# Performance work log

Measured on AMD Instinct MI355X. Metric: run time of the kernel, lower is better.

Reference implementation:

```python
import jax, jax.numpy as jnp
import numpy as np

N = 50000      # nodes
E = 800000     # edges (avg degree 16)
NFEAT = 256
NHID = 128
NCLASS = 40
NLAYERS_MID = 13  # gc2..gc14


def setup_inputs() -> dict:
    key = jax.random.key(0)
    ks = jax.random.split(key, 16)
    stdv_h = 1.0 / np.sqrt(NHID)     # GraphConvolution stdv = 1/sqrt(out_features)
    stdv_c = 1.0 / np.sqrt(NCLASS)
    u = lambda k, shape, s: jax.random.uniform(k, shape, jnp.float32, -s, s)
    return {
        "x": jax.random.normal(ks[0], (N, NFEAT), jnp.float32),
        "edge_src": jax.random.randint(ks[1], (E,), 0, N, jnp.int32),
        "edge_dst": jax.random.randint(ks[2], (E,), 0, N, jnp.int32),
        "edge_weight": jax.random.uniform(ks[3], (E,), jnp.float32),
        # skip-branch linear (self.weight / self.bias)
        "W0": u(ks[4], (NFEAT, NHID), stdv_h),
        "b0": u(ks[5], (NHID,), stdv_h),
        # gc1: nfeat -> nhid
        "W1": u(ks[6], (NFEAT, NHID), stdv_h),
        "b1": u(ks[7], (NHID,), stdv_h),
        # gc2..gc14: nhid -> nhid, stacked
        "Wmid": u(ks[8], (NLAYERS_MID, NHID, NHID), stdv_h),
        "bmid": u(ks[9], (NLAYERS_MID, NHID), stdv_h),
        # gc15: 14*nhid -> nclass
        "W15": u(ks[10], (14 * NHID, NCLASS), stdv_c),
        "b15": u(ks[11], (NCLASS,), stdv_c),
    }


def reference(x, edge_src, edge_dst, edge_weight, W0, b0, W1, b1, Wmid, bmid, W15, b15):
    n = x.shape[0]

    def gcn(h, W, b):
        # support = h @ W ; out = spmm(adj, support) + b  (adj as weighted edge list)
        support = h @ W
        msgs = support[edge_src] * edge_weight[:, None]           # [E, d]
        agg = jax.ops.segment_sum(msgs, edge_dst, num_segments=n)  # [N, d]
        return agg + b

    z = x @ W0 + b0
    x1 = jax.nn.relu(gcn(x, W1, b1)) + z

    def step(h, Wb):
        W, b = Wb
        hn = jax.nn.relu(gcn(h, W, b)) + h
        return hn, hn

    _, xs = jax.lax.scan(step, x1, (Wmid, bmid))   # xs: [13, N, NHID] = x2..x14
    all_x = jnp.concatenate([x1[None], xs], axis=0)  # [14, N, NHID] = x1..x14
    # concat order in torch code: (x14, x13, ..., x1)
    x_cat = jnp.swapaxes(all_x[::-1], 0, 1).reshape(n, 14 * NHID)
    # dropout is identity in eval mode
    x15 = gcn(x_cat, W15, b15)
    return jax.nn.log_softmax(x15, axis=1)
```

## Files before the change

### kernel.cpp

```cpp
#include <hip/hip_runtime.h>
#include <stdint.h>

#define NN 50000
#define EE 800000
#define DH 128
#define NC 40
#define KCAT (14*DH)
#define CAP 64

typedef __bf16 bf16x8 __attribute__((ext_vector_type(8)));
typedef float floatx4 __attribute__((ext_vector_type(4)));

__device__ __forceinline__ float bf2f(unsigned short u) {
  union { uint32_t i; float f; } v; v.i = ((uint32_t)u) << 16; return v.f;
}
__device__ __forceinline__ unsigned short f2bf(float f) {
  union { float f; uint32_t i; } v; v.f = f;
  uint32_t x = v.i;
  uint32_t r = (x + 0x7fffu + ((x >> 16) & 1u)) >> 16;
  return (unsigned short)r;
}

__global__ void zero_i32(int* p, int n) {
  int i = blockIdx.x * blockDim.x + threadIdx.x;
  if (i < n) p[i] = 0;
}

__global__ void detect_dtype(const unsigned short* xw, int* wildcnt) {
  int t = threadIdx.x;
  int wild = 0;
  for (int i = t; i < 4096; i += 256) {
    unsigned e = (xw[i] >> 7) & 0xFF;
    if (e >= 0x90) wild++;
  }
  if (wild) atomicAdd(wildcnt, wild);
}

__global__ void convert_f(const void* in, unsigned short* outp, int n, const int* flag) {
  bool isf32 = (*flag) > 32;
  for (int i = blockIdx.x * blockDim.x + threadIdx.x; i < n;
       i += gridDim.x * blockDim.x) {
    outp[i] = isf32 ? f2bf(((const float*)in)[i]) : ((const unsigned short*)in)[i];
  }
}

__global__ void transpose_w(const void* B, unsigned short* BT,
                            int L, int K, int M, int Mpad, const int* flag) {
  bool isf32 = (*flag) > 32;
  int total = L * Mpad * K;
  for (int idx = blockIdx.x * blockDim.x + threadIdx.x; idx < total;
       idx += gridDim.x * blockDim.x) {
    int k = idx % K;
    int n = (idx / K) % Mpad;
    int l = idx / (K * Mpad);
    unsigned short v = 0;
    if (n < M) {
      size_t si = (size_t)l * K * M + (size_t)k * M + n;
      v = isf32 ? f2bf(((const float*)B)[si]) : ((const unsigned short*)B)[si];
    }
    BT[idx] = v;
  }
}

__global__ void build_ell(const int* __restrict__ src, const int* __restrict__ dst,
                          const void* __restrict__ w,
                          int* __restrict__ cnt, int2* __restrict__ ell,
                          const int* __restrict__ flag) {
  bool isf32 = (*flag) > 32;
  int e = blockIdx.x * blockDim.x + threadIdx.x;
  if (e >= EE) return;
  int d = dst[e];
  if ((unsigned)d >= NN) return;
  int p = atomicAdd(&cnt[d], 1);
  if (p >= CAP) return;
  int s = src[e];
  float wf = isf32 ? ((const float*)w)[e] : bf2f(((const unsigned short*)w)[e]);
  if ((unsigned)s >= NN) { s = 0; wf = 0.f; }
  union { float f; int i; } wv; wv.f = wf;
  ell[(size_t)d * CAP + p] = make_int2(s, wv.i);
}

__global__ __launch_bounds__(256) void gemm_h(
    const unsigned short* __restrict__ A, int lda,
    const unsigned short* __restrict__ BT, int K,
    unsigned short* __restrict__ C, const unsigned short* __restrict__ bias) {
  __shared__ unsigned short As[128][40];
  __shared__ unsigned short Bs[128][40];
  int t = threadIdx.x;
  int wave = t >> 6, lane = t & 63;
  int wy = wave >> 1, wx = wave & 1;
  int q = lane >> 4, mn = lane & 15;
  int r0 = blockIdx.x * 128;
  floatx4 acc[4][4];
  floatx4 zf = {0.f, 0.f, 0.f, 0.f};
  #pragma unroll
  for (int i = 0; i < 4; ++i)
    #pragma unroll
    for (int j = 0; j < 4; ++j) acc[i][j] = zf;

  int arow = t >> 2;
  int akc = (t & 3) << 3;

  for (int k0 = 0; k0 < K; k0 += 32) {
    #pragma unroll
    for (int h = 0; h < 2; ++h) {
      int r = arow + h * 64;
      uint4 v = make_uint4(0, 0, 0, 0);
      if (r0 + r < NN) v = *(const uint4*)(A + (size_t)(r0 + r) * lda + k0 + akc);
      *(uint4*)(&As[r][akc]) = v;
    }
    #pragma unroll
    for (int h = 0; h < 2; ++h) {
      int n = arow + h * 64;
      uint4 v = *(const uint4*)(BT + (size_t)n * K + k0 + akc);
      *(uint4*)(&Bs[n][akc]) = v;
    }
    __syncthreads();
    bf16x8 fa[4], fb[4];
    #pragma unroll
    for (int i = 0; i < 4; ++i) fa[i] = *(const bf16x8*)(&As[wy * 64 + i * 16 + mn][q * 8]);
    #pragma unroll
    for (int j = 0; j < 4; ++j) fb[j] = *(const bf16x8*)(&Bs[wx * 64 + j * 16 + mn][q * 8]);
    #pragma unroll
    for (int i = 0; i < 4; ++i)
      #pragma unroll
      for (int j = 0; j < 4; ++j)
        acc[i][j] = __builtin_amdgcn_mfma_f32_16x16x32_bf16(fa[i], fb[j], acc[i][j], 0, 0, 0);
    __syncthreads();
  }
  #pragma unroll
  for (int i = 0; i < 4; ++i) {
    int rbase = r0 + wy * 64 + i * 16 + q * 4;
    #pragma unroll
    for (int j = 0; j < 4; ++j) {
      int col = wx * 64 + j * 16 + mn;
      float badd = bias ? bf2f(bias[col]) : 0.0f;
      #pragma unroll
      for (int rr = 0; rr < 4; ++rr) {
        int row = rbase + rr;
        if (row < NN) C[(size_t)row * 128 + col] = f2bf(acc[i][j][rr] + badd);
      }
    }
  }
}

__global__ __launch_bounds__(256) void gemm_cat(
    const unsigned short* __restrict__ A, const unsigned short* __restrict__ BT ,
    float* __restrict__ C) {
  __shared__ unsigned short As[128][40];
  __shared__ unsigned short Bs[48][40];
  int t = threadIdx.x;
  int wave = t >> 6, lane = t & 63;
  int q = lane >> 4, mn = lane & 15;
  int r0 = blockIdx.x * 128;
  floatx4 acc[2][3];
  floatx4 zf = {0.f, 0.f, 0.f, 0.f};
  #pragma unroll
  for (int i = 0; i < 2; ++i)
    #pragma unroll
    for (int j = 0; j < 3; ++j) acc[i][j] = zf;

  int arow = t >> 2;
  int akc = (t & 3) << 3;

  for (int k0 = 0; k0 < KCAT; k0 += 32) {
    #pragma unroll
    for (int h = 0; h < 2; ++h) {
      int r = arow + h * 64;
      uint4 v = make_uint4(0, 0, 0, 0);
      if (r0 + r < NN) v = *(const uint4*)(A + (size_t)(r0 + r) * KCAT + k0 + akc);
      *(uint4*)(&As[r][akc]) = v;
    }
    if (t < 192) {
      uint4 v = *(const uint4*)(BT + (size_t)arow * KCAT + k0 + akc);
      *(uint4*)(&Bs[arow][akc]) = v;
    }
    __syncthreads();
    bf16x8 fa[2], fb[3];
    #pragma unroll
    for (int i = 0; i < 2; ++i) fa[i] = *(const bf16x8*)(&As[wave * 32 + i * 16 + mn][q * 8]);
    #pragma unroll
    for (int j = 0; j < 3; ++j) fb[j] = *(const bf16x8*)(&Bs[j * 16 + mn][q * 8]);
    #pragma unroll
    for (int i = 0; i < 2; ++i)
      #pragma unroll
      for (int j = 0; j < 3; ++j)
        acc[i][j] = __builtin_amdgcn_mfma_f32_16x16x32_bf16(fa[i], fb[j], acc[i][j], 0, 0, 0);
    __syncthreads();
  }
  #pragma unroll
  for (int i = 0; i < 2; ++i) {
    int rbase = r0 + wave * 32 + i * 16 + q * 4;
    #pragma unroll
    for (int j = 0; j < 3; ++j) {
      int col = j * 16 + mn;
      #pragma unroll
      for (int rr = 0; rr < 4; ++rr) {
        int row = rbase + rr;
        if (row < NN && col < NC) C[(size_t)row * NC + col] = acc[i][j][rr];
      }
    }
  }
}

__global__ __launch_bounds__(256) void spmm_layer(
    const unsigned short* __restrict__ support, const int* __restrict__ cnt,
    const int2* __restrict__ ell, const unsigned short* __restrict__ bias,
    const unsigned short* __restrict__ res, int res_stride,
    unsigned short* __restrict__ out, int out_stride) {
  int wave = threadIdx.x >> 6, lane = threadIdx.x & 63;
  int row = blockIdx.x * 4 + wave;
  if (row >= NN) return;
  int n = cnt[row];
  if (n > CAP) n = CAP;
  int2 ev = ell[(size_t)row * CAP + lane];
  float a0 = 0.f, a1 = 0.f;
  int j = 0;
  for (; j + 8 <= n; j += 8) {
    uint32_t g[8];
    int sidx[8];
    #pragma unroll
    for (int u = 0; u < 8; ++u) sidx[u] = __shfl(ev.x, j + u);
    #pragma unroll
    for (int u = 0; u < 8; ++u)
      g[u] = *(const uint32_t*)(support + (size_t)sidx[u] * DH + 2 * lane);
    #pragma unroll
    for (int u = 0; u < 8; ++u) {
      union { int i; float f; } wv; wv.i = __shfl(ev.y, j + u);
      a0 += wv.f * bf2f((unsigned short)(g[u] & 0xffff));
      a1 += wv.f * bf2f((unsigned short)(g[u] >> 16));
    }
  }
  for (; j < n; ++j) {
    int s = __shfl(ev.x, j);
    union { int i; float f; } wv; wv.i = __shfl(ev.y, j);
    uint32_t g = *(const uint32_t*)(support + (size_t)s * DH + 2 * lane);
    a0 += wv.f * bf2f((unsigned short)(g & 0xffff));
    a1 += wv.f * bf2f((unsigned short)(g >> 16));
  }
  uint32_t bw = *(const uint32_t*)(bias + 2 * lane);
  uint32_t rw = *(const uint32_t*)(res + (size_t)row * res_stride + 2 * lane);
  float v0 = fmaxf(a0 + bf2f((unsigned short)(bw & 0xffff)), 0.f) +
             bf2f((unsigned short)(rw & 0xffff));
  float v1 = fmaxf(a1 + bf2f((unsigned short)(bw >> 16)), 0.f) +
             bf2f((unsigned short)(rw >> 16));
  uint32_t o = (uint32_t)f2bf(v0) | ((uint32_t)f2bf(v1) << 16);
  *(uint32_t*)(out + (size_t)row * out_stride + 2 * lane) = o;
}

__global__ __launch_bounds__(256) void spmm_softmax_out(
    const float* __restrict__ s15, const int* __restrict__ cnt,
    const int2* __restrict__ ell, const unsigned short* __restrict__ bias,
    float* __restrict__ out) {
  int wave = threadIdx.x >> 6, lane = threadIdx.x & 63;
  int row = blockIdx.x * 4 + wave;
  if (row >= NN) return;
  int n = cnt[row];
  if (n > CAP) n = CAP;
  int2 ev = ell[(size_t)row * CAP + lane];
  int fl = lane < NC ? lane : NC - 1;
  float acc = 0.f;
  int j = 0;
  for (; j + 4 <= n; j += 4) {
    float g[4];
    #pragma unroll
    for (int u = 0; u < 4; ++u) {
      int s = __shfl(ev.x, j + u);
      g[u] = s15[(size_t)s * NC + fl];
    }
    #pragma unroll
    for (int u = 0; u < 4; ++u) {
      union { int i; float f; } wv; wv.i = __shfl(ev.y, j + u);
      acc += wv.f * g[u];
    }
  }
  for (; j < n; ++j) {
    int s = __shfl(ev.x, j);
    union { int i; float f; } wv; wv.i = __shfl(ev.y, j);
    acc += wv.f * s15[(size_t)s * NC + fl];
  }
  acc += bf2f(bias[fl]);
  float v = (lane < NC) ? acc : -3.0e38f;
  float m = v;
  #pragma unroll
  for (int off = 32; off > 0; off >>= 1) m = fmaxf(m, __shfl_xor(m, off));
  float e = (lane < NC) ? expf(v - m) : 0.f;
  float sum = e;
  #pragma unroll
  for (int off = 32; off > 0; off >>= 1) sum += __shfl_xor(sum, off);
  if (lane < NC) out[(size_t)row * NC + lane] = v - m - logf(sum);
}

extern "C" void kernel_launch(void* const* d_in, const int* in_sizes, int n_in,
                              void* d_out, int out_size, void* d_ws, size_t ws_size,
                              hipStream_t stream) {
  const void* x   = d_in[0];
  const int* esrc = (const int*)d_in[1];
  const int* edst = (const int*)d_in[2];
  const void* ew  = d_in[3];
  const void* W0  = d_in[4];
  const void* b0  = d_in[5];
  const void* W1  = d_in[6];
  const void* b1  = d_in[7];
  const void* Wm  = d_in[8];
  const void* bm  = d_in[9];
  const void* W15 = d_in[10];
  const void* b15 = d_in[11];
  float* out = (float*)d_out;

  char* ws = (char*)d_ws;
  size_t off = 0;
  auto alloc = [&](size_t bytes) -> void* {
    void* p = ws + off;
    off = (off + bytes + 255) & ~(size_t)255;
    return p;
  };
  unsigned short* xcat = (unsigned short*)alloc((size_t)NN * KCAT * 2);
  unsigned short* xbf  = (unsigned short*)alloc((size_t)NN * 256 * 2);
  unsigned short* supp = (unsigned short*)alloc((size_t)NN * DH * 2);
  unsigned short* zbuf = (unsigned short*)alloc((size_t)NN * DH * 2);
  float* s15           = (float*)alloc((size_t)NN * NC * 4);
  int* counts          = (int*)alloc((size_t)(NN + 1) * 4);
  int2* ell            = (int2*)alloc((size_t)NN * CAP * 8);
  unsigned short* W0T  = (unsigned short*)alloc((size_t)256 * 128 * 2);
  unsigned short* W1T  = (unsigned short*)alloc((size_t)256 * 128 * 2);
  unsigned short* WmT  = (unsigned short*)alloc((size_t)13 * 128 * 128 * 2);
  unsigned short* W15T = (unsigned short*)alloc((size_t)48 * 1792 * 2);
  unsigned short* bb   = (unsigned short*)alloc((size_t)(128 + 128 + 13 * 128 + 40) * 2);
  if (off > ws_size) return;
  int* flag = counts + NN;
  unsigned short* b0b  = bb;
  unsigned short* b1b  = bb + 128;
  unsigned short* bmb  = bb + 256;
  unsigned short* b15b = bb + 256 + 13 * 128;

  zero_i32<<<197, 256, 0, stream>>>(counts, NN + 1);
  detect_dtype<<<1, 256, 0, stream>>>((const unsigned short*)x, flag);
  transpose_w<<<128, 256, 0, stream>>>(W0, W0T, 1, 256, 128, 128, flag);
  transpose_w<<<128, 256, 0, stream>>>(W1, W1T, 1, 256, 128, 128, flag);
  transpose_w<<<832, 256, 0, stream>>>(Wm, WmT, 13, 128, 128, 128, flag);
  transpose_w<<<336, 256, 0, stream>>>(W15, W15T, 1, 1792, 40, 48, flag);
  convert_f<<<2048, 256, 0, stream>>>(x, xbf, NN * 256, flag);
  convert_f<<<1, 128, 0, stream>>>(b0, b0b, 128, flag);
  convert_f<<<1, 128, 0, stream>>>(b1, b1b, 128, flag);
  convert_f<<<7, 256, 0, stream>>>(bm, bmb, 13 * 128, flag);
  convert_f<<<1, 64, 0, stream>>>(b15, b15b, 40, flag);
  build_ell<<<3125, 256, 0, stream>>>(esrc, edst, ew, counts, ell, flag);

  int gb = (NN + 127) / 128;
  int sb = (NN + 3) / 4;
  gemm_h<<<gb, 256, 0, stream>>>(xbf, 256, W0T, 256, zbuf, b0b);
  gemm_h<<<gb, 256, 0, stream>>>(xbf, 256, W1T, 256, supp, nullptr);
  spmm_layer<<<sb, 256, 0, stream>>>(supp, counts, ell, b1b, zbuf, DH,
                                     xcat + 13 * DH, KCAT);
  for (int l = 0; l < 13; ++l) {
    gemm_h<<<gb, 256, 0, stream>>>(xcat + (13 - l) * DH, KCAT, WmT + l * 128 * 128, 128,
                                   supp, nullptr);
    spmm_layer<<<sb, 256, 0, stream>>>(supp, counts, ell, bmb + l * DH,
                                       xcat + (13 - l) * DH, KCAT,
                                       xcat + (12 - l) * DH, KCAT);
  }
  gemm_cat<<<gb, 256, 0, stream>>>(xcat, W15T, s15);
  spmm_softmax_out<<<sb, 256, 0, stream>>>(s15, counts, ell, b15b, out);
}
```

Before: 965.9 us.

## Shrink GEMM row tiles, split-K the concat GEMM with atomics, guard ELL loads

The hidden GEMM now uses 64-row tiles, so there are twice as many blocks, and each wave owns a 32-column strip. The final 1792-wide concat GEMM is split four ways along K using a 2D grid, with results accumulated by atomicAdd into a pre-zeroed fp32 buffer. Shared-memory row padding changes from 40 to 72, and the SpMM kernels skip loading ELL entries beyond each row's count. The aim is more parallelism for the small-N GEMMs and less wasted ELL traffic, at the cost of an extra zeroing pass, float atomics with nondeterministic summation order, and reloading the B tile per block.

```diff
diff --git a/kernel.cpp b/kernel.cpp
--- a/kernel.cpp
+++ b/kernel.cpp
@@ -7,6 +7,7 @@
 #define NC 40
 #define KCAT (14*DH)
 #define CAP 64
+#define LP 72
 
 typedef __bf16 bf16x8 __attribute__((ext_vector_type(8)));
 typedef float floatx4 __attribute__((ext_vector_type(4)));
@@ -84,30 +85,27 @@
     const unsigned short* __restrict__ A, int lda,
     const unsigned short* __restrict__ BT, int K,
     unsigned short* __restrict__ C, const unsigned short* __restrict__ bias) {
-  __shared__ unsigned short As[128][40];
-  __shared__ unsigned short Bs[128][40];
+  __shared__ unsigned short As[64][LP];
+  __shared__ unsigned short Bs[128][LP];
   int t = threadIdx.x;
   int wave = t >> 6, lane = t & 63;
-  int wy = wave >> 1, wx = wave & 1;
   int q = lane >> 4, mn = lane & 15;
-  int r0 = blockIdx.x * 128;
-  floatx4 acc[4][4];
+  int r0 = blockIdx.x * 64;
+  floatx4 acc[4][2];
   floatx4 zf = {0.f, 0.f, 0.f, 0.f};
   #pragma unroll
   for (int i = 0; i < 4; ++i)
     #pragma unroll
-    for (int j = 0; j < 4; ++j) acc[i][j] = zf;
+    for (int j = 0; j < 2; ++j) acc[i][j] = zf;
 
   int arow = t >> 2;
   int akc = (t & 3) << 3;
 
   for (int k0 = 0; k0 < K; k0 += 32) {
-    #pragma unroll
-    for (int h = 0; h < 2; ++h) {
-      int r = arow + h * 64;
+    {
       uint4 v = make_uint4(0, 0, 0, 0);
-      if (r0 + r < NN) v = *(const uint4*)(A + (size_t)(r0 + r) * lda + k0 + akc);
-      *(uint4*)(&As[r][akc]) = v;
+      if (r0 + arow < NN) v = *(const uint4*)(A + (size_t)(r0 + arow) * lda + k0 + akc);
+      *(uint4*)(&As[arow][akc]) = v;
     }
     #pragma unroll
     for (int h = 0; h < 2; ++h) {
@@ -116,24 +114,24 @@
       *(uint4*)(&Bs[n][akc]) = v;
     }
     __syncthreads();
-    bf16x8 fa[4], fb[4];
-    #pragma unroll
-    for (int i = 0; i < 4; ++i) fa[i] = *(const bf16x8*)(&As[wy * 64 + i * 16 + mn][q * 8]);
-    #pragma unroll
-    for (int j = 0; j < 4; ++j) fb[j] = *(const bf16x8*)(&Bs[wx * 64 + j * 16 + mn][q * 8]);
+    bf16x8 fa[4], fb[2];
+    #pragma unroll
+    for (int i = 0; i < 4; ++i) fa[i] = *(const bf16x8*)(&As[i * 16 + mn][q * 8]);
+    #pragma unroll
+    for (int j = 0; j < 2; ++j) fb[j] = *(const bf16x8*)(&Bs[wave * 32 + j * 16 + mn][q * 8]);
     #pragma unroll
     for (int i = 0; i < 4; ++i)
       #pragma unroll
-      for (int j = 0; j < 4; ++j)
+      for (int j = 0; j < 2; ++j)
         acc[i][j] = __builtin_amdgcn_mfma_f32_16x16x32_bf16(fa[i], fb[j], acc[i][j], 0, 0, 0);
     __syncthreads();
   }
   #pragma unroll
   for (int i = 0; i < 4; ++i) {
-    int rbase = r0 + wy * 64 + i * 16 + q * 4;
-    #pragma unroll
-    for (int j = 0; j < 4; ++j) {
-      int col = wx * 64 + j * 16 + mn;
+    int rbase = r0 + i * 16 + q * 4;
+    #pragma unroll
+    for (int j = 0; j < 2; ++j) {
+      int col = wave * 32 + j * 16 + mn;
       float badd = bias ? bf2f(bias[col]) : 0.0f;
       #pragma unroll
       for (int rr = 0; rr < 4; ++rr) {
@@ -147,12 +145,13 @@
 __global__ __launch_bounds__(256) void gemm_cat(
     const unsigned short* __restrict__ A, const unsigned short* __restrict__ BT ,
     float* __restrict__ C) {
-  __shared__ unsigned short As[128][40];
-  __shared__ unsigned short Bs[48][40];
+  __shared__ unsigned short As[128][LP];
+  __shared__ unsigned short Bs[48][LP];
   int t = threadIdx.x;
   int wave = t >> 6, lane = t & 63;
   int q = lane >> 4, mn = lane & 15;
   int r0 = blockIdx.x * 128;
+  int kbeg = blockIdx.y * (KCAT / 4), kend = kbeg + KCAT / 4;
   floatx4 acc[2][3];
   floatx4 zf = {0.f, 0.f, 0.f, 0.f};
   #pragma unroll
@@ -163,7 +162,7 @@
   int arow = t >> 2;
   int akc = (t & 3) << 3;
 
-  for (int k0 = 0; k0 < KCAT; k0 += 32) {
+  for (int k0 = kbeg; k0 < kend; k0 += 32) {
     #pragma unroll
     for (int h = 0; h < 2; ++h) {
       int r = arow + h * 64;
@@ -197,7 +196,8 @@
       #pragma unroll
       for (int rr = 0; rr < 4; ++rr) {
         int row = rbase + rr;
-        if (row < NN && col < NC) C[(size_t)row * NC + col] = acc[i][j][rr];
+        if (row < NN && col < NC)
+          atomicAdd(&C[(size_t)row * NC + col], acc[i][j][rr]);
       }
     }
   }
@@ -213,7 +213,8 @@
   if (row >= NN) return;
   int n = cnt[row];
   if (n > CAP) n = CAP;
-  int2 ev = ell[(size_t)row * CAP + lane];
+  int2 ev = make_int2(0, 0);
+  if (lane < n) ev = ell[(size_t)row * CAP + lane];
   float a0 = 0.f, a1 = 0.f;
   int j = 0;
   for (; j + 8 <= n; j += 8) {
@@ -257,7 +258,8 @@
   if (row >= NN) return;
   int n = cnt[row];
   if (n > CAP) n = CAP;
-  int2 ev = ell[(size_t)row * CAP + lane];
+  int2 ev = make_int2(0, 0);
+  if (lane < n) ev = ell[(size_t)row * CAP + lane];
   int fl = lane < NC ? lane : NC - 1;
   float acc = 0.f;
   int j = 0;
@@ -335,6 +337,7 @@
   unsigned short* b15b = bb + 256 + 13 * 128;
 
   zero_i32<<<197, 256, 0, stream>>>(counts, NN + 1);
+  zero_i32<<<7813, 256, 0, stream>>>((int*)s15, NN * NC);
   detect_dtype<<<1, 256, 0, stream>>>((const unsigned short*)x, flag);
   transpose_w<<<128, 256, 0, stream>>>(W0, W0T, 1, 256, 128, 128, flag);
   transpose_w<<<128, 256, 0, stream>>>(W1, W1T, 1, 256, 128, 128, flag);
@@ -347,7 +350,7 @@
   convert_f<<<1, 64, 0, stream>>>(b15, b15b, 40, flag);
   build_ell<<<3125, 256, 0, stream>>>(esrc, edst, ew, counts, ell, flag);
 
-  int gb = (NN + 127) / 128;
+  int gb = (NN + 63) / 64;
   int sb = (NN + 3) / 4;
   gemm_h<<<gb, 256, 0, stream>>>(xbf, 256, W0T, 256, zbuf, b0b);
   gemm_h<<<gb, 256, 0, stream>>>(xbf, 256, W1T, 256, supp, nullptr);
@@ -360,6 +363,6 @@
                                        xcat + (13 - l) * DH, KCAT,
                                        xcat + (12 - l) * DH, KCAT);
   }
-  gemm_cat<<<gb, 256, 0, stream>>>(xcat, W15T, s15);
+  gemm_cat<<<dim3(391, 4), 256, 0, stream>>>(xcat, W15T, s15);
   spmm_softmax_out<<<sb, 256, 0, stream>>>(s15, counts, ell, b15b, out);
 }
```

After: 970.1 us. No clear change (+0.4%).
